# Kernel optimization log

Hardware: AMD Instinct MI355X
Metric: run time of the kernel (lower is better)

The kernel has to match this reference:

```python
import jax, jax.numpy as jnp
import numpy as np

B, T, F, H = 128, 1024, 64, 256


def _lstm_cell(x, h, c, W_ih, W_hh, b):
    # x: [B,F], h,c: [B,H]; gate order i,f,g,o (PyTorch convention)
    gates = x @ W_ih.T + h @ W_hh.T + b  # [B,4H]
    i, f, g, o = jnp.split(gates, 4, axis=-1)
    i, f, o = jax.nn.sigmoid(i), jax.nn.sigmoid(f), jax.nn.sigmoid(o)
    g = jnp.tanh(g)
    c = f * c + i * g
    h = o * jnp.tanh(c)
    return h, c


def setup_inputs() -> dict:
    key = jax.random.key(0)
    ks = jax.random.split(key, 10)
    s = 1.0 / np.sqrt(H)
    inp = {
        "ts_batch": jax.random.normal(ks[0], (B, T, F), jnp.float32),
        "W_ih_enc": jax.random.uniform(ks[1], (4 * H, F), jnp.float32, -s, s),
        "W_hh_enc": jax.random.uniform(ks[2], (4 * H, H), jnp.float32, -s, s),
        "b_enc": jax.random.uniform(ks[3], (4 * H,), jnp.float32, -s, s),
        "W_ih_dec": jax.random.uniform(ks[4], (4 * H, F), jnp.float32, -s, s),
        "W_hh_dec": jax.random.uniform(ks[5], (4 * H, H), jnp.float32, -s, s),
        "b_dec": jax.random.uniform(ks[6], (4 * H,), jnp.float32, -s, s),
        "W_out": jax.random.uniform(ks[7], (F, H), jnp.float32, -s, s),
        "b_out": jax.random.uniform(ks[8], (F,), jnp.float32, -s, s),
    }
    return inp


def reference(ts_batch, W_ih_enc, W_hh_enc, b_enc, W_ih_dec, W_hh_dec, b_dec, W_out, b_out):
    batch = ts_batch.shape[0]
    hidden = W_hh_enc.shape[1]
    xs = jnp.swapaxes(ts_batch, 0, 1)  # [T,B,F]

    # ---- encoder: full-sequence LSTM, keep only final (h,c) ----
    def enc_step(carry, x):
        h, c = carry
        h, c = _lstm_cell(x, h, c, W_ih_enc, W_hh_enc, b_enc)
        return (h, c), None

    h0 = jnp.zeros((batch, hidden), ts_batch.dtype)
    (h, c), _ = jax.lax.scan(enc_step, (h0, h0), xs)

    # ---- decoder: iterate timesteps in reverse; emit projection of the
    # hidden state BEFORE consuming the input at that step (training branch) ----
    def dec_step(carry, x):
        h, c = carry
        out = h @ W_out.T + b_out  # [B,F]
        h, c = _lstm_cell(x, h, c, W_ih_dec, W_hh_dec, b_dec)
        return (h, c), out

    _, outs_rev = jax.lax.scan(dec_step, (h, c), xs[::-1])  # [T,B,F], reversed time
    return jnp.swapaxes(outs_rev[::-1], 0, 1)  # [B,T,F]
```

## Files before the change

### kernel.cpp

```cpp
#include <hip/hip_runtime.h>
#include <hip/hip_bf16.h>


#define Bb 128
#define Tt 1024
#define Ff 64
#define Hh 256

typedef _Float16 h16;
typedef __attribute__((ext_vector_type(8))) _Float16 h16x8;
typedef __attribute__((ext_vector_type(4))) float f32x4;
typedef unsigned long long u64;

#define WENC_OFF 0
#define WDEC_OFF 327680
#define WOUT_OFF 655360
#define HBUF_OFF 671744
#define FLAGS_BYTE_OFF 1474560

__device__ __forceinline__ float fast_sigmoid(float x) {
  float e = __expf(-fabsf(x));
  float s = __builtin_amdgcn_rcpf(1.f + e);
  return x >= 0.f ? s : 1.f - s;
}
__device__ __forceinline__ float fast_tanh(float x) {
  float e = __expf(-2.f * fabsf(x));
  float r = (1.f - e) * __builtin_amdgcn_rcpf(1.f + e);
  return x >= 0.f ? r : -r;
}
__device__ __forceinline__ h16x8 pack16(u64 lo, u64 hi) {
  union { u64 u[2]; h16x8 v; } x;
  x.u[0] = lo; x.u[1] = hi;
  return x.v;
}

__global__ void lstm_prep(const float* __restrict__ Wih_e, const float* __restrict__ Whh_e,
                          const float* __restrict__ Wih_d, const float* __restrict__ Whh_d,
                          const float* __restrict__ Wout, h16* __restrict__ ws16,
                          unsigned int* __restrict__ flags) {
  int e = blockIdx.x * 256 + threadIdx.x;
  if (e < 256) flags[e] = 0u;
  if (e < 655360) {
    int r = e;
    const float* Wih = Wih_e; const float* Whh = Whh_e;
    int off = WENC_OFF;
    if (r >= 327680) { r -= 327680; Wih = Wih_d; Whh = Whh_d; off = WDEC_OFF; }
    int j    = r & 7;
    int lane = (r >> 3) & 63;
    int kt   = (r >> 9) % 10;
    int tmp  = (r >> 9) / 10;
    int nt   = tmp & 7;
    int w    = (tmp >> 3) & 3;
    int q    = tmp >> 5;
    int g = nt >> 1, ct = nt & 1;
    int col = q * 128 + w * 32 + ct * 16 + (lane & 15);
    int row = g * 256 + col;
    int k = kt * 32 + (lane >> 4) * 8 + j;
    float v = (k < 64) ? Wih[row * 64 + k] : Whh[row * 256 + (k - 64)];
    ws16[off + r] = (h16)v;
  } else if (e < 655360 + 16384) {
    int r = e - 655360;
    int j    = r & 7;
    int lane = (r >> 3) & 63;
    int kt   = (r >> 9) & 7;
    int wt   = (r >> 12) & 1;
    int q    = (r >> 13) & 1;
    int f = q * 32 + wt * 16 + (lane & 15);
    int k = kt * 32 + (lane >> 4) * 8 + j;
    ws16[WOUT_OFF + r] = (h16)Wout[f * 256 + k];
  }
}

#define MFMA_KT(kt) do {                                                         \
    acc[0] = __builtin_amdgcn_mfma_f32_16x16x32_f16(a[kt], wf[0][kt], acc[0], 0, 0, 0); \
    acc[1] = __builtin_amdgcn_mfma_f32_16x16x32_f16(a[kt], wf[1][kt], acc[1], 0, 0, 0); \
    acc[2] = __builtin_amdgcn_mfma_f32_16x16x32_f16(a[kt], wf[2][kt], acc[2], 0, 0, 0); \
    acc[3] = __builtin_amdgcn_mfma_f32_16x16x32_f16(a[kt], wf[3][kt], acc[3], 0, 0, 0); \
    acc[4] = __builtin_amdgcn_mfma_f32_16x16x32_f16(a[kt], wf[4][kt], acc[4], 0, 0, 0); \
    acc[5] = __builtin_amdgcn_mfma_f32_16x16x32_f16(a[kt], wf[5][kt], acc[5], 0, 0, 0); \
    acc[6] = __builtin_amdgcn_mfma_f32_16x16x32_f16(a[kt], wf[6][kt], acc[6], 0, 0, 0); \
    acc[7] = __builtin_amdgcn_mfma_f32_16x16x32_f16(a[kt], wf[7][kt], acc[7], 0, 0, 0); \
  } while (0)

__global__ __launch_bounds__(256, 1) void lstm_main(
    const float* __restrict__ ts,
    const float* __restrict__ b_enc, const float* __restrict__ b_dec,
    const float* __restrict__ b_out,
    const h16* __restrict__ wsW, h16* __restrict__ hbuf,
    unsigned int* flags, float* __restrict__ out) {
  const int tid = threadIdx.x;
  const int wg = blockIdx.x;
  const int grp = wg & 7, q = wg >> 3;
  const int w = tid >> 6, lane = tid & 63;
  const int n16 = lane & 15, quad = lane >> 4;
  const int b0 = grp * 16;
  const int partner = wg ^ 8;

  __shared__ __align__(16) h16 xh[2][16][328];
  __shared__ h16x8 woutLds[1024];

  h16x8 wf[8][10];
  {
    const h16x8* wsrc = (const h16x8*)(wsW + WENC_OFF);
#pragma unroll
    for (int nt = 0; nt < 8; ++nt)
#pragma unroll
      for (int kt = 0; kt < 10; ++kt)
        wf[nt][kt] = wsrc[(((q * 4 + w) * 8 + nt) * 10 + kt) * 64 + lane];
  }
  float bias8[8];
#pragma unroll
  for (int nt = 0; nt < 8; ++nt) {
    int g = nt >> 1, ct = nt & 1;
    bias8[nt] = b_enc[g * 256 + q * 128 + w * 32 + ct * 16 + n16];
  }
  const float bo = b_out[q * 32 + w * 16 + n16];

  float c8[8];
#pragma unroll
  for (int i = 0; i < 8; ++i) c8[i] = 0.f;

  for (int i = tid; i < 16 * 264; i += 256) {
    int m = i / 264;
    xh[0][m][64 + (i - m * 264)] = (h16)0.f;
  }
  const int m_x = tid >> 4, ks_x = (tid & 15) * 4;
  {
    const f32x4 xv0 = *(const f32x4*)(ts + ((size_t)(b0 + m_x) * Tt + 0) * Ff + ks_x);
#pragma unroll
    for (int u = 0; u < 4; ++u) xh[0][m_x][ks_x + u] = (h16)xv0[u];
  }
  __syncthreads();

  for (int t = 0; t < 2048; ++t) {
    const int nb = t & 1, nxt = nb ^ 1;
    const bool dec = (t >= 1024);

    if (t == 1024) {
      const h16x8* wsrc2 = (const h16x8*)(wsW + WDEC_OFF);
#pragma unroll
      for (int nt = 0; nt < 8; ++nt)
#pragma unroll
        for (int kt = 0; kt < 10; ++kt)
          wf[nt][kt] = wsrc2[(((q * 4 + w) * 8 + nt) * 10 + kt) * 64 + lane];
#pragma unroll
      for (int nt = 0; nt < 8; ++nt) {
        int g = nt >> 1, ct = nt & 1;
        bias8[nt] = b_dec[g * 256 + q * 128 + w * 32 + ct * 16 + n16];
      }
      const h16x8* wo = (const h16x8*)(wsW + WOUT_OFF) + q * 1024;
      for (int i = tid; i < 1024; i += 256) woutLds[i] = wo[i];
      __syncthreads();
    }

    h16x8 a[10];
    const h16* xrow = &xh[nb][n16][0];
    a[0] = *(const h16x8*)(xrow + 0 * 32 + quad * 8);
    a[1] = *(const h16x8*)(xrow + 1 * 32 + quad * 8);
    if (q == 0) {
      a[2] = *(const h16x8*)(xrow + 2 * 32 + quad * 8);
      a[3] = *(const h16x8*)(xrow + 3 * 32 + quad * 8);
      a[4] = *(const h16x8*)(xrow + 4 * 32 + quad * 8);
      a[5] = *(const h16x8*)(xrow + 5 * 32 + quad * 8);
    } else {
      a[6] = *(const h16x8*)(xrow + 6 * 32 + quad * 8);
      a[7] = *(const h16x8*)(xrow + 7 * 32 + quad * 8);
      a[8] = *(const h16x8*)(xrow + 8 * 32 + quad * 8);
      a[9] = *(const h16x8*)(xrow + 9 * 32 + quad * 8);
    }

    f32x4 acc[8];
#pragma unroll
    for (int nt = 0; nt < 8; ++nt) {
      f32x4 v; v[0] = bias8[nt]; v[1] = bias8[nt]; v[2] = bias8[nt]; v[3] = bias8[nt];
      acc[nt] = v;
    }
    MFMA_KT(0); MFMA_KT(1);
    if (q == 0) { MFMA_KT(2); MFMA_KT(3); MFMA_KT(4); MFMA_KT(5); }
    else        { MFMA_KT(6); MFMA_KT(7); MFMA_KT(8); MFMA_KT(9); }

    f32x4 xv;
#pragma unroll
    for (int u = 0; u < 4; ++u) xv[u] = 0.f;
    if (t + 1 < 2048) {
      int xi = (t + 1 < 1024) ? (t + 1) : (2047 - (t + 1));
      xv = *(const f32x4*)(ts + ((size_t)(b0 + m_x) * Tt + xi) * Ff + ks_x);
    }

    if (t > 0) {
      const unsigned int need = 4u * (unsigned int)t;
      while (__hip_atomic_load(&flags[partner * 16], __ATOMIC_RELAXED,
                               __HIP_MEMORY_SCOPE_AGENT) < need) { }
      asm volatile("" ::: "memory");
      const u64* ps64 = (const u64*)hbuf + ((size_t)partner * 2 + nxt) * 512;
      const int jb = (n16 * 16 + quad) * 2;
      u64 dl0 = __hip_atomic_load((u64*)(ps64 + jb + 0),  __ATOMIC_RELAXED, __HIP_MEMORY_SCOPE_AGENT);
      u64 dh0 = __hip_atomic_load((u64*)(ps64 + jb + 1),  __ATOMIC_RELAXED, __HIP_MEMORY_SCOPE_AGENT);
      u64 dl1 = __hip_atomic_load((u64*)(ps64 + jb + 8),  __ATOMIC_RELAXED, __HIP_MEMORY_SCOPE_AGENT);
      u64 dh1 = __hip_atomic_load((u64*)(ps64 + jb + 9),  __ATOMIC_RELAXED, __HIP_MEMORY_SCOPE_AGENT);
      u64 dl2 = __hip_atomic_load((u64*)(ps64 + jb + 16), __ATOMIC_RELAXED, __HIP_MEMORY_SCOPE_AGENT);
      u64 dh2 = __hip_atomic_load((u64*)(ps64 + jb + 17), __ATOMIC_RELAXED, __HIP_MEMORY_SCOPE_AGENT);
      u64 dl3 = __hip_atomic_load((u64*)(ps64 + jb + 24), __ATOMIC_RELAXED, __HIP_MEMORY_SCOPE_AGENT);
      u64 dh3 = __hip_atomic_load((u64*)(ps64 + jb + 25), __ATOMIC_RELAXED, __HIP_MEMORY_SCOPE_AGENT);
      if (q == 0) {
        a[6] = pack16(dl0, dh0); a[7] = pack16(dl1, dh1);
        a[8] = pack16(dl2, dh2); a[9] = pack16(dl3, dh3);
        MFMA_KT(6); MFMA_KT(7); MFMA_KT(8); MFMA_KT(9);
      } else {
        a[2] = pack16(dl0, dh0); a[3] = pack16(dl1, dh1);
        a[4] = pack16(dl2, dh2); a[5] = pack16(dl3, dh3);
        MFMA_KT(2); MFMA_KT(3); MFMA_KT(4); MFMA_KT(5);
      }
    }

    h16 hv[8];
#pragma unroll
    for (int ct = 0; ct < 2; ++ct)
#pragma unroll
      for (int r = 0; r < 4; ++r) {
        float i_ = fast_sigmoid(acc[0 + ct][r]);
        float f_ = fast_sigmoid(acc[2 + ct][r]);
        float g_ = fast_tanh(acc[4 + ct][r]);
        float o_ = fast_sigmoid(acc[6 + ct][r]);
        float cv = f_ * c8[ct * 4 + r] + i_ * g_;
        c8[ct * 4 + r] = cv;
        hv[ct * 4 + r] = (h16)(o_ * fast_tanh(cv));
      }

#pragma unroll
    for (int ct = 0; ct < 2; ++ct)
#pragma unroll
      for (int r = 0; r < 4; ++r) {
        int m = quad * 4 + r;
        int colLocal = w * 32 + ct * 16 + n16;
        xh[nxt][m][64 + q * 128 + colLocal] = hv[ct * 4 + r];
      }
    if (t + 1 < 2048) {
#pragma unroll
      for (int u = 0; u < 4; ++u) xh[nxt][m_x][ks_x + u] = (h16)xv[u];
    }

    __syncthreads();

    if (t < 2047) {
      u64* hb64 = (u64*)hbuf + ((size_t)wg * 2 + nb) * 512;
#pragma unroll
      for (int r2 = 0; r2 < 2; ++r2) {
        const int k = tid + r2 * 256;
        const int mm = k >> 5, c4 = k & 31;
        u64 v = *(const u64*)(&xh[nxt][mm][64 + q * 128 + c4 * 4]);
        __hip_atomic_store(hb64 + k, v, __ATOMIC_RELAXED, __HIP_MEMORY_SCOPE_AGENT);
      }
      asm volatile("s_waitcnt vmcnt(0)" ::: "memory");
      if (lane == 0)
        __hip_atomic_fetch_add(&flags[wg * 16], 1u, __ATOMIC_RELAXED,
                               __HIP_MEMORY_SCOPE_AGENT);
    }

    if (dec && w < 2) {
      f32x4 ao; ao[0] = bo; ao[1] = bo; ao[2] = bo; ao[3] = bo;
#pragma unroll
      for (int kt = 0; kt < 8; ++kt)
        ao = __builtin_amdgcn_mfma_f32_16x16x32_f16(a[2 + kt], woutLds[(w * 8 + kt) * 64 + lane], ao, 0, 0, 0);
      int tpos = 2047 - t;
      int f = q * 32 + w * 16 + n16;
#pragma unroll
      for (int r = 0; r < 4; ++r) {
        int m = quad * 4 + r;
        out[((size_t)(b0 + m) * Tt + tpos) * Ff + f] = ao[r];
      }
    }
  }
}

extern "C" void kernel_launch(void* const* d_in, const int* in_sizes, int n_in,
                              void* d_out, int out_size, void* d_ws, size_t ws_size,
                              hipStream_t stream) {
  const float* ts  = (const float*)d_in[0];
  const float* Wie = (const float*)d_in[1];
  const float* Whe = (const float*)d_in[2];
  const float* be  = (const float*)d_in[3];
  const float* Wid = (const float*)d_in[4];
  const float* Whd = (const float*)d_in[5];
  const float* bd  = (const float*)d_in[6];
  const float* Wo  = (const float*)d_in[7];
  const float* bo  = (const float*)d_in[8];

  h16* ws16 = (h16*)d_ws;
  unsigned int* flags = (unsigned int*)((char*)d_ws + FLAGS_BYTE_OFF);
  float* out = (float*)d_out;

  lstm_prep<<<2624, 256, 0, stream>>>(Wie, Whe, Wid, Whd, Wo, ws16, flags);
  lstm_main<<<16, 256, 0, stream>>>(ts, be, bd, bo, ws16, ws16 + HBUF_OFF, flags, out);
}
```

Baseline: 9.076 ms.

## Replace flag counter handshake with per-word timestep-tagged hidden state exchange

Each 16-bit hidden value is now stored in a 32-bit word whose upper half carries the timestep tag. The consumer polls the data words directly until every tag matches. This removes the separate flag atomic, the vmcnt wait and the counter poll, cutting one round trip per step on the cross-workgroup critical path. In exchange the exchanged data doubles in size, more loads are issued per poll iteration, and the loads are issued before the local MFMAs to overlap latency.

```diff
diff --git a/kernel.cpp b/kernel.cpp
--- a/kernel.cpp
+++ b/kernel.cpp
@@ -11,12 +11,13 @@
 typedef __attribute__((ext_vector_type(8))) _Float16 h16x8;
 typedef __attribute__((ext_vector_type(4))) float f32x4;
 typedef unsigned long long u64;
+typedef unsigned int u32;
 
 #define WENC_OFF 0
 #define WDEC_OFF 327680
 #define WOUT_OFF 655360
-#define HBUF_OFF 671744
 #define FLAGS_BYTE_OFF 1474560
+#define TAGHB_BYTE_OFF 1475584
 
 __device__ __forceinline__ float fast_sigmoid(float x) {
   float e = __expf(-fabsf(x));
@@ -32,6 +33,12 @@
   union { u64 u[2]; h16x8 v; } x;
   x.u[0] = lo; x.u[1] = hi;
   return x.v;
+}
+__device__ __forceinline__ u64 detag2(u64 p, u64 q) {
+  u32 w0 = (u32)p, w1 = (u32)(p >> 32), w2 = (u32)q, w3 = (u32)(q >> 32);
+  u32 lo = (w0 & 0xFFFFu) | (w1 << 16);
+  u32 hi = (w2 & 0xFFFFu) | (w3 << 16);
+  return (u64)lo | ((u64)hi << 32);
 }
 
 __global__ void lstm_prep(const float* __restrict__ Wih_e, const float* __restrict__ Whh_e,
@@ -40,6 +47,10 @@
                           unsigned int* __restrict__ flags) {
   int e = blockIdx.x * 256 + threadIdx.x;
   if (e < 256) flags[e] = 0u;
+  if (e < 65536) {
+    u32* tag32 = flags + 256;
+    tag32[e] = 0xFFFF0000u;
+  }
   if (e < 655360) {
     int r = e;
     const float* Wih = Wih_e; const float* Whh = Whh_e;
@@ -82,12 +93,23 @@
     acc[7] = __builtin_amdgcn_mfma_f32_16x16x32_f16(a[kt], wf[7][kt], acc[7], 0, 0, 0); \
   } while (0)
 
+#define LOAD16() do {                                                            \
+    _Pragma("unroll")                                                            \
+    for (int ii = 0; ii < 8; ++ii) {                                             \
+      const int bi = 2 * (jb + OFFS[ii]);                                        \
+      tg[2 * ii]     = __hip_atomic_load(tb + bi,     __ATOMIC_RELAXED,          \
+                                         __HIP_MEMORY_SCOPE_AGENT);              \
+      tg[2 * ii + 1] = __hip_atomic_load(tb + bi + 1, __ATOMIC_RELAXED,          \
+                                         __HIP_MEMORY_SCOPE_AGENT);              \
+    }                                                                            \
+  } while (0)
+
 __global__ __launch_bounds__(256, 1) void lstm_main(
     const float* __restrict__ ts,
     const float* __restrict__ b_enc, const float* __restrict__ b_dec,
     const float* __restrict__ b_out,
-    const h16* __restrict__ wsW, h16* __restrict__ hbuf,
-    unsigned int* flags, float* __restrict__ out) {
+    const h16* __restrict__ wsW, u64* __restrict__ tagbuf,
+    float* __restrict__ out) {
   const int tid = threadIdx.x;
   const int wg = blockIdx.x;
   const int grp = wg & 7, q = wg >> 3;
@@ -131,6 +153,9 @@
     for (int u = 0; u < 4; ++u) xh[0][m_x][ks_x + u] = (h16)xv0[u];
   }
   __syncthreads();
+
+  static const int OFFS[8] = {0, 1, 8, 9, 16, 17, 24, 25};
+  const int jb = (n16 * 16 + quad) * 2;
 
   for (int t = 0; t < 2048; ++t) {
     const int nb = t & 1, nxt = nb ^ 1;
@@ -169,6 +194,10 @@
       a[9] = *(const h16x8*)(xrow + 9 * 32 + quad * 8);
     }
 
+    const u64* tb = tagbuf + ((size_t)partner * 2 + nxt) * 1024;
+    u64 tg[16];
+    if (t > 0) LOAD16();
+
     f32x4 acc[8];
 #pragma unroll
     for (int nt = 0; nt < 8; ++nt) {
@@ -188,27 +217,30 @@
     }
 
     if (t > 0) {
-      const unsigned int need = 4u * (unsigned int)t;
-      while (__hip_atomic_load(&flags[partner * 16], __ATOMIC_RELAXED,
-                               __HIP_MEMORY_SCOPE_AGENT) < need) { }
-      asm volatile("" ::: "memory");
-      const u64* ps64 = (const u64*)hbuf + ((size_t)partner * 2 + nxt) * 512;
-      const int jb = (n16 * 16 + quad) * 2;
-      u64 dl0 = __hip_atomic_load((u64*)(ps64 + jb + 0),  __ATOMIC_RELAXED, __HIP_MEMORY_SCOPE_AGENT);
-      u64 dh0 = __hip_atomic_load((u64*)(ps64 + jb + 1),  __ATOMIC_RELAXED, __HIP_MEMORY_SCOPE_AGENT);
-      u64 dl1 = __hip_atomic_load((u64*)(ps64 + jb + 8),  __ATOMIC_RELAXED, __HIP_MEMORY_SCOPE_AGENT);
-      u64 dh1 = __hip_atomic_load((u64*)(ps64 + jb + 9),  __ATOMIC_RELAXED, __HIP_MEMORY_SCOPE_AGENT);
-      u64 dl2 = __hip_atomic_load((u64*)(ps64 + jb + 16), __ATOMIC_RELAXED, __HIP_MEMORY_SCOPE_AGENT);
-      u64 dh2 = __hip_atomic_load((u64*)(ps64 + jb + 17), __ATOMIC_RELAXED, __HIP_MEMORY_SCOPE_AGENT);
-      u64 dl3 = __hip_atomic_load((u64*)(ps64 + jb + 24), __ATOMIC_RELAXED, __HIP_MEMORY_SCOPE_AGENT);
-      u64 dh3 = __hip_atomic_load((u64*)(ps64 + jb + 25), __ATOMIC_RELAXED, __HIP_MEMORY_SCOPE_AGENT);
+      const u64 tmask = 0xFFFF0000FFFF0000ull;
+      const u64 texp = ((u64)(u32)t << 48) | ((u64)(u32)t << 16);
+      for (;;) {
+        bool ok = true;
+#pragma unroll
+        for (int ii = 0; ii < 16; ++ii) ok &= ((tg[ii] & tmask) == texp);
+        if (ok) break;
+        LOAD16();
+      }
+      u64 d0 = detag2(tg[0],  tg[1]);
+      u64 d1 = detag2(tg[2],  tg[3]);
+      u64 d2 = detag2(tg[4],  tg[5]);
+      u64 d3 = detag2(tg[6],  tg[7]);
+      u64 d4 = detag2(tg[8],  tg[9]);
+      u64 d5 = detag2(tg[10], tg[11]);
+      u64 d6 = detag2(tg[12], tg[13]);
+      u64 d7 = detag2(tg[14], tg[15]);
       if (q == 0) {
-        a[6] = pack16(dl0, dh0); a[7] = pack16(dl1, dh1);
-        a[8] = pack16(dl2, dh2); a[9] = pack16(dl3, dh3);
+        a[6] = pack16(d0, d1); a[7] = pack16(d2, d3);
+        a[8] = pack16(d4, d5); a[9] = pack16(d6, d7);
         MFMA_KT(6); MFMA_KT(7); MFMA_KT(8); MFMA_KT(9);
       } else {
-        a[2] = pack16(dl0, dh0); a[3] = pack16(dl1, dh1);
-        a[4] = pack16(dl2, dh2); a[5] = pack16(dl3, dh3);
+        a[2] = pack16(d0, d1); a[3] = pack16(d2, d3);
+        a[4] = pack16(d4, d5); a[5] = pack16(d6, d7);
         MFMA_KT(2); MFMA_KT(3); MFMA_KT(4); MFMA_KT(5);
       }
     }
@@ -243,18 +275,18 @@
     __syncthreads();
 
     if (t < 2047) {
-      u64* hb64 = (u64*)hbuf + ((size_t)wg * 2 + nb) * 512;
+      u64* pb = tagbuf + ((size_t)wg * 2 + nb) * 1024;
+      const u32 tagw = (u32)(t + 1) << 16;
 #pragma unroll
       for (int r2 = 0; r2 < 2; ++r2) {
         const int k = tid + r2 * 256;
-        const int mm = k >> 5, c4 = k & 31;
-        u64 v = *(const u64*)(&xh[nxt][mm][64 + q * 128 + c4 * 4]);
-        __hip_atomic_store(hb64 + k, v, __ATOMIC_RELAXED, __HIP_MEMORY_SCOPE_AGENT);
-      }
-      asm volatile("s_waitcnt vmcnt(0)" ::: "memory");
-      if (lane == 0)
-        __hip_atomic_fetch_add(&flags[wg * 16], 1u, __ATOMIC_RELAXED,
-                               __HIP_MEMORY_SCOPE_AGENT);
+        u64 v = *(const u64*)(&xh[nxt][k >> 5][64 + q * 128 + (k & 31) * 4]);
+        u32 lo = (u32)v, hi = (u32)(v >> 32);
+        u64 tglo = (u64)(tagw | (lo & 0xFFFFu)) | ((u64)(tagw | (lo >> 16)) << 32);
+        u64 tghi = (u64)(tagw | (hi & 0xFFFFu)) | ((u64)(tagw | (hi >> 16)) << 32);
+        __hip_atomic_store(pb + 2 * k,     tglo, __ATOMIC_RELAXED, __HIP_MEMORY_SCOPE_AGENT);
+        __hip_atomic_store(pb + 2 * k + 1, tghi, __ATOMIC_RELAXED, __HIP_MEMORY_SCOPE_AGENT);
+      }
     }
 
     if (dec && w < 2) {
@@ -288,8 +320,9 @@
 
   h16* ws16 = (h16*)d_ws;
   unsigned int* flags = (unsigned int*)((char*)d_ws + FLAGS_BYTE_OFF);
+  u64* tagbuf = (u64*)((char*)d_ws + TAGHB_BYTE_OFF);
   float* out = (float*)d_out;
 
   lstm_prep<<<2624, 256, 0, stream>>>(Wie, Whe, Wid, Whd, Wo, ws16, flags);
-  lstm_main<<<16, 256, 0, stream>>>(ts, be, bd, bo, ws16, ws16 + HBUF_OFF, flags, out);
-}
+  lstm_main<<<16, 256, 0, stream>>>(ts, be, bd, bo, ws16, tagbuf, out);
+}
```

Result: slower. 12.24 ms (+34.9%).
